# Performance work log

Measured on AMD Instinct MI355X. Metric: run time of the kernel, lower is better.

The kernel has to match this reference:

```python
import jax, jax.numpy as jnp
import numpy as np

B, C, CO, H, W = 64, 64, 64, 56, 56
E, K = 8, 2


def _conv3x3(x, k, b):
    # x: [B,C,H,W], k: [CO,C,3,3], b: [CO]
    y = jax.lax.conv_general_dilated(
        x, k, window_strides=(1, 1), padding='SAME',
        dimension_numbers=('NCHW', 'OIHW', 'NCHW'))
    return y + b[None, :, None, None]


def setup_inputs() -> dict:
    key = jax.random.key(0)
    k1, k2, k3, k4, k5 = jax.random.split(key, 5)
    x = jax.random.normal(k1, (B, C, H, W), dtype=jnp.float32)
    weights = jax.random.uniform(k2, (B, K), dtype=jnp.float32)
    indices = jax.random.randint(k3, (B, K), 0, E, dtype=jnp.int32)
    W_exp = jax.random.normal(k4, (E, CO, C, 3, 3), dtype=jnp.float32) * 0.05
    b_exp = jax.random.normal(k5, (E, CO), dtype=jnp.float32) * 0.01
    return {'x': x, 'weights': weights, 'indices': indices,
            'W_exp': W_exp, 'b_exp': b_exp}


def reference(x, weights, indices, W_exp, b_exp):
    # Dense-equivalent MoE dispatch: run every expert on the full batch,
    # then gather the top-k expert outputs per sample and combine.
    # Same math as the masked gather / index_add_ loop in the torch module.
    # acts: [E, B, CO, H, W]
    acts = jax.vmap(lambda k, b: jax.nn.relu(_conv3x3(x, k, b)))(W_exp, b_exp)
    acts_b = jnp.transpose(acts, (1, 0, 2, 3, 4))  # [B, E, CO, H, W]
    idx = indices[:, :, None, None, None].astype(jnp.int32)
    sel = jnp.take_along_axis(acts_b, idx, axis=1)  # [B, K, CO, H, W]
    out = jnp.sum(sel * weights[:, :, None, None, None], axis=1)  # [B, CO, H, W]
    return out
```

## Files before the change

### kernel.cpp

```cpp
#include <hip/hip_runtime.h>


#define BB 64
#define CC 64
#define COO 64
#define HH 56
#define WW 56

typedef __bf16 bf16x8 __attribute__((ext_vector_type(8)));
typedef float  f32x4  __attribute__((ext_vector_type(4)));

__global__ __launch_bounds__(256) void prep_kernel(
    const float* __restrict__ x, const float* __restrict__ Wexp,
    __bf16* __restrict__ xT, __bf16* __restrict__ Wpack)
{
    const int bx  = blockIdx.x;
    const int tid = threadIdx.x;

    if (bx < 960) {
        __shared__ float tile[CC][WW + 1];
        const int b   = bx / 15;
        const int grp = bx - b * 15;
        #pragma unroll 1
        for (int rr = 0; rr < 4; ++rr) {
            const int hp = grp * 4 + rr;
            if (hp >= 58) break;
            __bf16* dst = xT + ((size_t)b * 58 + hp) * 4224;
            const bool interior = (hp >= 1 && hp <= HH);
            if (!interior) {
                bf16x8 z = {};
                for (int j = tid; j < 4224 / 8; j += 256)
                    *(bf16x8*)(dst + j * 8) = z;
                continue;
            }
            const int h = hp - 1;
            const float* xb = x + (size_t)b * CC * HH * WW + (size_t)h * WW;
            for (int i = tid; i < CC * 14; i += 256) {
                const int c = i / 14, wq = i - c * 14;
                const float4 f = *(const float4*)(xb + (size_t)c * HH * WW + wq * 4);
                tile[c][wq * 4 + 0] = f.x; tile[c][wq * 4 + 1] = f.y;
                tile[c][wq * 4 + 2] = f.z; tile[c][wq * 4 + 3] = f.w;
            }
            __syncthreads();
            for (int j = tid; j < 66 * 8; j += 256) {
                const int cg = j / 66;
                const int wc = j - cg * 66;
                bf16x8 v = {};
                if (wc >= 1 && wc <= WW) {
                    const int w = wc - 1;
                    #pragma unroll
                    for (int u = 0; u < 8; ++u)
                        v[u] = (__bf16)tile[cg * 8 + u][w];
                }
                *(bf16x8*)(dst + j * 8) = v;
            }
            __syncthreads();
        }
    } else {
        const int wp = bx - 960;
        const int e  = wp / 9, rs = wp - e * 9;
        const int r  = rs / 3, s  = rs - r * 3;
        for (int idx = tid; idx < 4096; idx += 256) {
            const int ks   = idx >> 11;
            const int rem  = idx & 2047;
            const int mt   = rem >> 9;
            const int lane = (rem >> 3) & 63;
            const int j    = idx & 7;
            const int co = mt * 16 + (lane & 15);
            const int c  = ks * 32 + ((lane >> 4) << 3) + j;
            const float v = Wexp[((((size_t)e * COO + co) * CC + c) * 3 + r) * 3 + s];
            Wpack[(size_t)e * 36864 + (size_t)rs * 4096 + idx] = (__bf16)v;
        }
    }
}

__global__ __launch_bounds__(256, 3) void moe_conv_mfma(
    const __bf16* __restrict__ xT, const __bf16* __restrict__ Wpack,
    const float* __restrict__ gate_w, const int* __restrict__ gate_i,
    const float* __restrict__ bexp, float* __restrict__ out)
{
    __shared__ __align__(16) __bf16 ldsA[2 * 4096];

    const int bid = blockIdx.x;
    const int swz = (bid & 7) * 224 + (bid >> 3);
    const int b   = swz / 28;
    const int rem = swz - b * 28;
    const int h0  = (rem >> 1) * 4;
    const int mh  = rem & 1;

    const int tid = threadIdx.x;
    const int wid = tid >> 6, lane = tid & 63;
    const int n15 = lane & 15, quad = lane >> 4;
    const int wcol = wid * 16 + n15;

    const int   e0 = gate_i[b * 2 + 0], e1 = gate_i[b * 2 + 1];
    const float g0 = gate_w[b * 2 + 0], g1 = gate_w[b * 2 + 1];
    const __bf16* w0 = Wpack + (size_t)e0 * 36864;
    const __bf16* w1 = Wpack + (size_t)e1 * 36864;

    auto stage = [&](int rsn, int bufn) {
        #pragma unroll
        for (int i = 0; i < 2; ++i) {
            const __bf16* src = (wid >= 2 ? w1 : w0) + (size_t)rsn * 4096
                              + (wid & 1) * 2048 + (mh * 2 + i) * 512 + lane * 8;
            __bf16* dstp = &ldsA[bufn * 4096 + (wid * 2 + i) * 512 + lane * 8];
            __builtin_amdgcn_global_load_lds(
                (const __attribute__((address_space(1))) unsigned int*)src,
                (__attribute__((address_space(3))) unsigned int*)dstp, 16, 0, 0);
        }
    };

    const __bf16* pq = xT + (size_t)b * 244992 + quad * 528 + wcol * 8;

    f32x4  acc[2][2][4] = {};
    bf16x8 bfb[2][2][4];

    auto loadB = [&](int rsn, int pf) {
        const int rn = rsn / 3, sn = rsn - rn * 3;
        const __bf16* pb = pq + (size_t)(h0 + rn) * 4224 + sn * 8;
        #pragma unroll
        for (int ks = 0; ks < 2; ++ks)
            #pragma unroll
            for (int t = 0; t < 4; ++t)
                bfb[pf][ks][t] = *(const bf16x8*)(pb + t * 4224 + ks * 2112);
    };

    stage(0, 0);
    loadB(0, 0);
    #pragma unroll
    for (int rs = 0; rs < 9; ++rs) {
        const int buf = rs & 1;
        __syncthreads();
        if (rs < 8) {
            stage(rs + 1, buf ^ 1);
            loadB(rs + 1, buf ^ 1);
        }
        #pragma unroll
        for (int ks = 0; ks < 2; ++ks) {
            #pragma unroll
            for (int slot = 0; slot < 2; ++slot) {
                #pragma unroll
                for (int mtl = 0; mtl < 2; ++mtl) {
                    const bf16x8 af = *(const bf16x8*)
                        &ldsA[buf * 4096 + slot * 2048 + ks * 1024 + mtl * 512 + lane * 8];
                    #pragma unroll
                    for (int t = 0; t < 4; ++t)
                        acc[slot][mtl][t] = __builtin_amdgcn_mfma_f32_16x16x32_bf16(
                            af, bfb[buf][ks][t], acc[slot][mtl][t], 0, 0, 0);
                }
            }
        }
    }

    if (wcol < WW) {
        #pragma unroll
        for (int t = 0; t < 4; ++t) {
            const int h = h0 + t;
            #pragma unroll
            for (int mtl = 0; mtl < 2; ++mtl) {
                #pragma unroll
                for (int v = 0; v < 4; ++v) {
                    const int co = (mh * 2 + mtl) * 16 + quad * 4 + v;
                    float a0 = acc[0][mtl][t][v] + bexp[e0 * COO + co];
                    float a1 = acc[1][mtl][t][v] + bexp[e1 * COO + co];
                    a0 = fmaxf(a0, 0.f);
                    a1 = fmaxf(a1, 0.f);
                    out[(((size_t)b * COO + co) * HH + h) * WW + wcol] =
                        g0 * a0 + g1 * a1;
                }
            }
        }
    }
}

extern "C" void kernel_launch(void* const* d_in, const int* in_sizes, int n_in,
                              void* d_out, int out_size, void* d_ws, size_t ws_size,
                              hipStream_t stream) {
    const float* x      = (const float*)d_in[0];
    const float* gate_w = (const float*)d_in[1];
    const int*   gate_i = (const int*)  d_in[2];
    const float* Wexp   = (const float*)d_in[3];
    const float* bexp   = (const float*)d_in[4];
    float* out = (float*)d_out;

    __bf16* Wpack = (__bf16*)d_ws;
    __bf16* xT    = (__bf16*)((char*)d_ws + 589824);

    prep_kernel<<<dim3(1032), 256, 0, stream>>>(x, Wexp, xT, Wpack);
    moe_conv_mfma<<<dim3(1792), 256, 0, stream>>>(xT, Wpack, gate_w, gate_i,
                                                  bexp, out);
}
```

Before: 146.3 us.

## Triple-buffer conv pipeline with manual waitcnt, single barrier and MFMA priority

Replaces the double-buffered LDS/register pipeline with a three-stage ring. Weight tiles and input fragments are prefetched two filter taps ahead using inline-asm global loads, and completion is tracked with explicit vmcnt waits, leaving one barrier per iteration. Wave priority is raised around the MFMA block. The aim is to hide global-load latency behind the matrix math, at the cost of more LDS and registers, so occupancy drops from three blocks per SM to two. The manual vmcnt counting is fragile if the compiler emits other memory operations.

```diff
diff --git a/kernel.cpp b/kernel.cpp
--- a/kernel.cpp
+++ b/kernel.cpp
@@ -74,12 +74,12 @@
     }
 }
 
-__global__ __launch_bounds__(256, 3) void moe_conv_mfma(
+__global__ __launch_bounds__(256, 2) void moe_conv_mfma(
     const __bf16* __restrict__ xT, const __bf16* __restrict__ Wpack,
     const float* __restrict__ gate_w, const int* __restrict__ gate_i,
     const float* __restrict__ bexp, float* __restrict__ out)
 {
-    __shared__ __align__(16) __bf16 ldsA[2 * 4096];
+    __shared__ __align__(16) __bf16 ldsA[3 * 4096];
 
     const int bid = blockIdx.x;
     const int swz = (bid & 7) * 224 + (bid >> 3);
@@ -110,31 +110,45 @@
         }
     };
 
-    const __bf16* pq = xT + (size_t)b * 244992 + quad * 528 + wcol * 8;
-
-    f32x4  acc[2][2][4] = {};
-    bf16x8 bfb[2][2][4];
-
-    auto loadB = [&](int rsn, int pf) {
-        const int rn = rsn / 3, sn = rsn - rn * 3;
-        const __bf16* pb = pq + (size_t)(h0 + rn) * 4224 + sn * 8;
+    const __bf16* pqh = xT + (size_t)b * 244992 + (size_t)h0 * 4224
+                      + quad * 528 + wcol * 8;
+
+    f32x4 acc[2][2][4] = {};
+    f32x4 bfb[3][2][4];
+
+    auto issueB = [&](int m) {
+        const int rn = m / 3, sn = m - rn * 3, mb = m % 3;
         #pragma unroll
         for (int ks = 0; ks < 2; ++ks)
             #pragma unroll
-            for (int t = 0; t < 4; ++t)
-                bfb[pf][ks][t] = *(const bf16x8*)(pb + t * 4224 + ks * 2112);
+            for (int t = 0; t < 4; ++t) {
+                const __bf16* a = pqh + (size_t)(rn + t) * 4224 + sn * 8
+                                + ks * 2112;
+                asm volatile("global_load_dwordx4 %0, %1, off"
+                             : "=&v"(bfb[mb][ks][t]) : "v"(a));
+            }
     };
 
-    stage(0, 0);
-    loadB(0, 0);
+    stage(0, 0); issueB(0);
+    stage(1, 1); issueB(1);
+    asm volatile("s_waitcnt vmcnt(10)" ::: "memory");
+    __builtin_amdgcn_sched_barrier(0);
+    __builtin_amdgcn_s_barrier();
+    __builtin_amdgcn_sched_barrier(0);
+
     #pragma unroll
     for (int rs = 0; rs < 9; ++rs) {
-        const int buf = rs & 1;
-        __syncthreads();
-        if (rs < 8) {
-            stage(rs + 1, buf ^ 1);
-            loadB(rs + 1, buf ^ 1);
-        }
+        const int cbuf = rs % 3;
+        if (rs <= 6) {
+            stage(rs + 2, (rs + 2) % 3);
+            issueB(rs + 2);
+            asm volatile("s_waitcnt vmcnt(10)" ::: "memory");
+        } else if (rs == 7) {
+            asm volatile("s_waitcnt vmcnt(0)" ::: "memory");
+        }
+        __builtin_amdgcn_sched_barrier(0);
+
+        __builtin_amdgcn_s_setprio(1);
         #pragma unroll
         for (int ks = 0; ks < 2; ++ks) {
             #pragma unroll
@@ -142,13 +156,22 @@
                 #pragma unroll
                 for (int mtl = 0; mtl < 2; ++mtl) {
                     const bf16x8 af = *(const bf16x8*)
-                        &ldsA[buf * 4096 + slot * 2048 + ks * 1024 + mtl * 512 + lane * 8];
+                        &ldsA[cbuf * 4096 + slot * 2048 + ks * 1024 + mtl * 512
+                              + lane * 8];
+                    const bf16x8 bv = __builtin_bit_cast(bf16x8, bfb[cbuf][ks * 4 / 4][0]);
                     #pragma unroll
                     for (int t = 0; t < 4; ++t)
                         acc[slot][mtl][t] = __builtin_amdgcn_mfma_f32_16x16x32_bf16(
-                            af, bfb[buf][ks][t], acc[slot][mtl][t], 0, 0, 0);
+                            af, __builtin_bit_cast(bf16x8, bfb[cbuf][ks][t]),
+                            acc[slot][mtl][t], 0, 0, 0);
                 }
             }
+        }
+        __builtin_amdgcn_s_setprio(0);
+
+        if (rs < 8) {
+            __builtin_amdgcn_s_barrier();
+            __builtin_amdgcn_sched_barrier(0);
         }
     }
 
```

Result: no change. 148.7 us (+1.7%).
